# Kernel optimization log

Measured on AMD Instinct MI355X. Metric: run time of the kernel, lower is better.

The kernel has to match this reference:

```python
import jax, jax.numpy as jnp
import numpy as np

DIM = 512
HEADS = 4
HEAD_DIM = DIM // HEADS
HIDDEN = DIM * 2
DEPTH = 4
N = 32768
T = 4  # fixed branch/token dim


def _layernorm(x, w, b, eps=1e-5):
    m = jnp.mean(x, axis=-1, keepdims=True)
    v = jnp.mean(jnp.square(x - m), axis=-1, keepdims=True)
    return (x - m) * jax.lax.rsqrt(v + eps) * w + b


def setup_inputs() -> dict:
    key = jax.random.key(0)
    ks = jax.random.split(key, 24)
    s = 0.02
    d = {
        'x': jax.random.normal(ks[0], (N, DIM, T), dtype=jnp.float32),
        'branch_embed': s * jax.random.normal(ks[1], (T, DIM), dtype=jnp.float32),
        'ln1_w': jnp.ones((DEPTH, DIM), jnp.float32),
        'ln1_b': jnp.zeros((DEPTH, DIM), jnp.float32),
        'qkv_w': s * jax.random.normal(ks[2], (DEPTH, 3 * DIM, DIM), dtype=jnp.float32),
        'qkv_b': jnp.zeros((DEPTH, 3 * DIM), jnp.float32),
        'proj_w': s * jax.random.normal(ks[3], (DEPTH, DIM, DIM), dtype=jnp.float32),
        'proj_b': jnp.zeros((DEPTH, DIM), jnp.float32),
        'ln2_w': jnp.ones((DEPTH, DIM), jnp.float32),
        'ln2_b': jnp.zeros((DEPTH, DIM), jnp.float32),
        'ffn_w1': s * jax.random.normal(ks[4], (DEPTH, HIDDEN, DIM), dtype=jnp.float32),
        'ffn_b1': jnp.zeros((DEPTH, HIDDEN), jnp.float32),
        'ffn_w2': s * jax.random.normal(ks[5], (DEPTH, DIM, HIDDEN), dtype=jnp.float32),
        'ffn_b2': jnp.zeros((DEPTH, DIM), jnp.float32),
        'pool_q': s * jax.random.normal(ks[6], (DIM,), dtype=jnp.float32),
        'pool_w': s * jax.random.normal(ks[7], (DIM, DIM), dtype=jnp.float32),
        'out_ln_w': jnp.ones((DIM,), jnp.float32),
        'out_ln_b': jnp.zeros((DIM,), jnp.float32),
        'out_w1': s * jax.random.normal(ks[8], (DIM // 2, DIM), dtype=jnp.float32),
        'out_b1': jnp.zeros((DIM // 2,), jnp.float32),
        'out_w2': s * jax.random.normal(ks[9], (1, DIM // 2), dtype=jnp.float32),
        'out_b2': jnp.zeros((1,), jnp.float32),
    }
    return d


def reference(x, branch_embed, ln1_w, ln1_b, qkv_w, qkv_b, proj_w, proj_b,
              ln2_w, ln2_b, ffn_w1, ffn_b1, ffn_w2, ffn_b2,
              pool_q, pool_w, out_ln_w, out_ln_b, out_w1, out_b1, out_w2, out_b2):
    # (N, C, 4) -> (N, 4, C), add branch embedding
    x = jnp.swapaxes(x, 1, 2) + branch_embed[None]
    n = x.shape[0]
    scale = 1.0 / np.sqrt(HEAD_DIM)
    for i in range(DEPTH):
        # --- MHSA (pre-LN, eval mode -> dropout off) ---
        h = _layernorm(x, ln1_w[i], ln1_b[i])
        qkv = jnp.einsum('ntd,ed->nte', h, qkv_w[i]) + qkv_b[i]  # (N, T, 3D)
        q, k, v = jnp.split(qkv, 3, axis=-1)
        q = q.reshape(n, T, HEADS, HEAD_DIM).transpose(0, 2, 1, 3)
        k = k.reshape(n, T, HEADS, HEAD_DIM).transpose(0, 2, 1, 3)
        v = v.reshape(n, T, HEADS, HEAD_DIM).transpose(0, 2, 1, 3)
        scores = jnp.einsum('nhqd,nhkd->nhqk', q, k) * scale
        attn = jax.nn.softmax(scores, axis=-1)
        o = jnp.einsum('nhqk,nhkd->nhqd', attn, v)
        o = o.transpose(0, 2, 1, 3).reshape(n, T, DIM)
        o = jnp.einsum('ntd,ed->nte', o, proj_w[i]) + proj_b[i]
        x = x + o
        # --- FFN ---
        h = _layernorm(x, ln2_w[i], ln2_b[i])
        f = jax.nn.gelu(jnp.einsum('ntd,hd->nth', h, ffn_w1[i]) + ffn_b1[i], approximate=False)
        f = jnp.einsum('nth,dh->ntd', f, ffn_w2[i]) + ffn_b2[i]
        x = x + f
    # --- attention pooling head ---
    k = jnp.einsum('ntd,ed->nte', x, pool_w)            # pool_proj (no bias)
    score = jax.nn.softmax(jnp.einsum('d,ntd->nt', pool_q, k) / np.sqrt(DIM), axis=-1)
    z = jnp.einsum('nt,ntd->nd', score, x)
    z = _layernorm(z, out_ln_w, out_ln_b)
    z = jax.nn.gelu(z @ out_w1.T + out_b1, approximate=False)
    y = (z @ out_w2.T + out_b2)[:, 0]
    return y
```

## Files before the change

kernel.cpp:

```cpp
#include <hip/hip_runtime.h>

typedef unsigned short u16;
typedef unsigned int u32;
typedef __attribute__((ext_vector_type(8))) short s16x8;
typedef __attribute__((ext_vector_type(8))) unsigned short u16x8;
typedef __attribute__((ext_vector_type(4))) float f32x4;
typedef __attribute__((ext_vector_type(4))) unsigned int u32x4;

__device__ __forceinline__ u16 f2bf(float f) {
    u32 u = __float_as_uint(f);
    u32 r = (u + 0x7fffu + ((u >> 16) & 1u)) >> 16;
    return (u16)r;
}
__device__ __forceinline__ float bf2f(u16 u) { return __uint_as_float(((u32)u) << 16); }
__device__ __forceinline__ float bflo(u32 u) { return __uint_as_float(u << 16); }
__device__ __forceinline__ float bfhi(u32 u) { return __uint_as_float(u & 0xffff0000u); }
__device__ __forceinline__ float gelu_exact(float v) {
    return 0.5f * v * (1.0f + erff(v * 0.70710678118654752f));
}

__device__ __forceinline__ void gload16(const void* g, void* l) {
    __builtin_amdgcn_global_load_lds(
        (const __attribute__((address_space(1))) u32*)g,
        (__attribute__((address_space(3))) u32*)l, 16, 0, 0);
}

__global__ __launch_bounds__(256) void k_cvt6(const float* __restrict__ s0, u16* __restrict__ d0,
                                              const float* __restrict__ s1, u16* __restrict__ d1,
                                              const float* __restrict__ s2, u16* __restrict__ d2,
                                              const float* __restrict__ s3, u16* __restrict__ d3,
                                              const float* __restrict__ s4, u16* __restrict__ d4,
                                              const float* __restrict__ s5, u16* __restrict__ d5) {
    int i = blockIdx.x * 256 + threadIdx.x;
    const float* s; u16* d; int off;
    if (i < 786432)       { s = s0; d = d0; off = i; }
    else if (i < 1048576) { s = s1; d = d1; off = i - 786432; }
    else if (i < 1572864) { s = s2; d = d2; off = i - 1048576; }
    else if (i < 2097152) { s = s3; d = d3; off = i - 1572864; }
    else if (i < 2162688) { s = s4; d = d4; off = i - 2097152; }
    else                  { s = s5; d = d5; off = i - 2162688; }
    float4 v = *(const float4*)(s + (size_t)off * 4);
    u16 o0 = f2bf(v.x), o1 = f2bf(v.y), o2 = f2bf(v.z), o3 = f2bf(v.w);
    uint2 o; o.x = (u32)o0 | ((u32)o1 << 16); o.y = (u32)o2 | ((u32)o3 << 16);
    *(uint2*)(d + (size_t)off * 4) = o;
}

__global__ __launch_bounds__(256) void k_embed_ln(const float* __restrict__ x,
                                                  const float* __restrict__ be,
                                                  const float* __restrict__ w,
                                                  const float* __restrict__ b,
                                                  u16* __restrict__ Xb,
                                                  u16* __restrict__ Hb) {
    __shared__ u16 ld[4][512];
    int s = blockIdx.x;
    int tid = threadIdx.x;
    const float* xs = x + (size_t)s * 2048;
#pragma unroll
    for (int i = 0; i < 2; ++i) {
        int d = tid + i * 256;
        float4 v = *(const float4*)(xs + d * 4);
        ld[0][d] = f2bf(v.x + be[d]);
        ld[1][d] = f2bf(v.y + be[512 + d]);
        ld[2][d] = f2bf(v.z + be[1024 + d]);
        ld[3][d] = f2bf(v.w + be[1536 + d]);
    }
    __syncthreads();
    int t = tid >> 6, lane = tid & 63;
    u16x8 raw = *(const u16x8*)(&ld[t][lane * 8]);
    *(u16x8*)(Xb + ((size_t)s * 4 + t) * 512 + lane * 8) = raw;
    float a[8];
#pragma unroll
    for (int j = 0; j < 8; ++j) a[j] = bf2f(raw[j]);
    float s1 = 0.f, s2 = 0.f;
#pragma unroll
    for (int j = 0; j < 8; ++j) { s1 += a[j]; s2 += a[j] * a[j]; }
#pragma unroll
    for (int d = 1; d < 64; d <<= 1) { s1 += __shfl_xor(s1, d); s2 += __shfl_xor(s2, d); }
    float mean = s1 * (1.0f / 512.0f);
    float var  = s2 * (1.0f / 512.0f) - mean * mean;
    float rstd = rsqrtf(var + 1e-5f);
    float4 w0 = *(const float4*)(w + lane * 8);
    float4 w1 = *(const float4*)(w + lane * 8 + 4);
    float4 b0 = *(const float4*)(b + lane * 8);
    float4 b1 = *(const float4*)(b + lane * 8 + 4);
    float wv[8] = {w0.x, w0.y, w0.z, w0.w, w1.x, w1.y, w1.z, w1.w};
    float bv[8] = {b0.x, b0.y, b0.z, b0.w, b1.x, b1.y, b1.z, b1.w};
    u16x8 o;
#pragma unroll
    for (int j = 0; j < 8; ++j) o[j] = f2bf((a[j] - mean) * rstd * wv[j] + bv[j]);
    *(u16x8*)(Hb + ((size_t)s * 4 + t) * 512 + lane * 8) = o;
}

__global__ __launch_bounds__(256) void k_ln(const u16* __restrict__ Xb,
                                            const float* __restrict__ w,
                                            const float* __restrict__ b,
                                            u16* __restrict__ H) {
    int row = blockIdx.x * 4 + (threadIdx.x >> 6);
    int lane = threadIdx.x & 63;
    u16x8 xv = *(const u16x8*)(Xb + (size_t)row * 512 + lane * 8);
    float a[8];
#pragma unroll
    for (int j = 0; j < 8; ++j) a[j] = bf2f(xv[j]);
    float s1 = 0.f, s2 = 0.f;
#pragma unroll
    for (int j = 0; j < 8; ++j) { s1 += a[j]; s2 += a[j] * a[j]; }
#pragma unroll
    for (int d = 1; d < 64; d <<= 1) { s1 += __shfl_xor(s1, d); s2 += __shfl_xor(s2, d); }
    float mean = s1 * (1.0f / 512.0f);
    float var  = s2 * (1.0f / 512.0f) - mean * mean;
    float rstd = rsqrtf(var + 1e-5f);
    float4 w0 = *(const float4*)(w + lane * 8);
    float4 w1 = *(const float4*)(w + lane * 8 + 4);
    float4 b0 = *(const float4*)(b + lane * 8);
    float4 b1 = *(const float4*)(b + lane * 8 + 4);
    float wv[8] = {w0.x, w0.y, w0.z, w0.w, w1.x, w1.y, w1.z, w1.w};
    float bv[8] = {b0.x, b0.y, b0.z, b0.w, b1.x, b1.y, b1.z, b1.w};
    u16x8 o;
#pragma unroll
    for (int j = 0; j < 8; ++j) o[j] = f2bf((a[j] - mean) * rstd * wv[j] + bv[j]);
    *(u16x8*)(H + (size_t)row * 512 + lane * 8) = o;
}

template <bool BIAS, bool GELU_, bool RESID, bool BOUNCE, bool NT>
__global__ __launch_bounds__(512, 2) void k_gemm256(const u16* __restrict__ A,
                                                    const u16* __restrict__ W,
                                                    const float* __restrict__ bias,
                                                    u16* __restrict__ Cb,
                                                    u16* __restrict__ Xbres,
                                                    int K, int ncols, int TN, int T) {
    __shared__ __align__(16) u16 lds[2 * 32768];
    __shared__ __align__(16) u16 bounce[8192];
    int tid = threadIdx.x;
    int lane = tid & 63;
    int wid = tid >> 6;
    int G = gridDim.x, b = blockIdx.x;
    int start, end, step;
    if ((G & 7) == 0) {
        int xcd = b & 7, nxb = G >> 3, j = b >> 3;
        start = (int)(((long long)xcd * T) >> 3) + j;
        end   = (int)(((long long)(xcd + 1) * T) >> 3);
        step  = nxb;
    } else {
        start = (int)(((long long)b * T) / G);
        end   = (int)(((long long)(b + 1) * T) / G);
        step  = 1;
    }
    if (start >= end) return;
    int NS = K >> 6;
    int mgrp = wid >> 2, ngrp = wid & 3;

    f32x4 acc[8][4];
#pragma unroll
    for (int i = 0; i < 8; ++i)
#pragma unroll
        for (int j = 0; j < 4; ++j) acc[i][j] = (f32x4){0.f, 0.f, 0.f, 0.f};

    int srow = tid >> 3;
    int sel  = (((tid & 7) * 16) ^ ((srow & 7) << 4)) >> 1;
    size_t K64 = (size_t)K * 64;
    char* ldsB = (char*)lds;
    int wdst = wid * 1024;

    const u16 *cA0, *cA1, *cB0, *cB1, *nA0, *nA1, *nB0, *nB1;
    int cm0, cn0, nm0, nn0;
    auto tilePtrs = [&](int ti, const u16*& a0, const u16*& a1,
                        const u16*& b0, const u16*& b1, int& m0o, int& n0o) {
        int bx = ti / TN, by = ti - bx * TN;
        int m0 = bx * 256, n0 = by * 256;
        a0 = A + (size_t)(m0 + srow) * K + sel;
        a1 = A + (size_t)(m0 + 128 + srow) * K + sel;
        b0 = W + (size_t)(n0 + srow) * K + sel;
        b1 = W + (size_t)(n0 + 128 + srow) * K + sel;
        m0o = m0; n0o = n0;
    };

    auto S_Aq12 = [&](const u16* a0, const u16* a1, int s) {
        char* d = ldsB + (s & 1) * 65536 + wdst;
        gload16(a0 + (size_t)s * 64, d);
        gload16(a1 + (size_t)s * 64, d + 16384);
    };
    auto S_Aq34 = [&](const u16* a0, const u16* a1, int s) {
        char* d = ldsB + (s & 1) * 65536 + 8192 + wdst;
        gload16(a0 + K64 + (size_t)s * 64, d);
        gload16(a1 + K64 + (size_t)s * 64, d + 16384);
    };
    auto S_Blo = [&](const u16* b0, int s) {
        char* d = ldsB + (s & 1) * 65536 + 32768 + wdst;
        gload16(b0 + (size_t)s * 64, d);
        gload16(b0 + K64 + (size_t)s * 64, d + 8192);
    };
    auto S_Bhi = [&](const u16* b1, int s) {
        char* d = ldsB + (s & 1) * 65536 + 49152 + wdst;
        gload16(b1 + (size_t)s * 64, d);
        gload16(b1 + K64 + (size_t)s * 64, d + 8192);
    };

    int arow = mgrp * 128 + (lane & 15);
    int brow = ngrp * 64 + (lane & 15);
    int sub = (lane >> 4) << 4;
    int amask = ((arow & 7) << 4), bmask = ((brow & 7) << 4);
    int aoff0 = arow * 128 + (sub ^ amask);
    int boff0 = 32768 + brow * 128 + (sub ^ bmask);
    int aoff1 = arow * 128 + ((sub | 64) ^ amask);
    int boff1 = 32768 + brow * 128 + ((sub | 64) ^ bmask);

    tilePtrs(start, cA0, cA1, cB0, cB1, cm0, cn0);
    S_Blo(cB0, 0); S_Bhi(cB1, 0); S_Aq12(cA0, cA1, 0); S_Aq34(cA0, cA1, 0);
    S_Blo(cB0, 1); S_Bhi(cB1, 1); S_Aq12(cA0, cA1, 1);
    asm volatile("s_waitcnt vmcnt(6)" ::: "memory");
    __builtin_amdgcn_s_barrier();

    for (int ti = start; ti < end; ti += step) {
        bool hasNext = (ti + step < end);
        if (hasNext) tilePtrs(ti + step, nA0, nA1, nB0, nB1, nm0, nn0);

        s16x8 bfr[4][2];
        for (int s = 0; s < NS; ++s) {
            const char* sb = ldsB + (s & 1) * 65536;
            int st = s + 1, st2 = s + 2;
            bool n1 = st < NS, n2 = st2 < NS;
            s16x8 af[2][2];
#pragma unroll
            for (int ni = 0; ni < 4; ++ni) {
                bfr[ni][0] = *(const s16x8*)(sb + boff0 + ni * 2048);
                bfr[ni][1] = *(const s16x8*)(sb + boff1 + ni * 2048);
            }
            af[0][0] = *(const s16x8*)(sb + aoff0);
            af[0][1] = *(const s16x8*)(sb + aoff1);
            af[1][0] = *(const s16x8*)(sb + aoff0 + 2048);
            af[1][1] = *(const s16x8*)(sb + aoff1 + 2048);
            if (n1) S_Aq34(cA0, cA1, st); else if (hasNext) S_Aq34(nA0, nA1, st - NS);
            __builtin_amdgcn_s_barrier();
            __builtin_amdgcn_s_setprio(1);
#pragma unroll
            for (int mj = 0; mj < 2; ++mj)
#pragma unroll
                for (int ni = 0; ni < 4; ++ni) {
                    acc[mj][ni] = __builtin_amdgcn_mfma_f32_16x16x32_bf16(bfr[ni][0], af[mj][0], acc[mj][ni], 0, 0, 0);
                    acc[mj][ni] = __builtin_amdgcn_mfma_f32_16x16x32_bf16(bfr[ni][1], af[mj][1], acc[mj][ni], 0, 0, 0);
                }
            __builtin_amdgcn_s_setprio(0);
            __builtin_amdgcn_s_barrier();
#pragma unroll
            for (int mj = 0; mj < 2; ++mj) {
                af[mj][0] = *(const s16x8*)(sb + aoff0 + (2 + mj) * 2048);
                af[mj][1] = *(const s16x8*)(sb + aoff1 + (2 + mj) * 2048);
            }
            if (n2) S_Blo(cB0, st2); else if (hasNext) S_Blo(nB0, st2 - NS);
            __builtin_amdgcn_s_barrier();
            __builtin_amdgcn_s_setprio(1);
#pragma unroll
            for (int mj = 0; mj < 2; ++mj)
#pragma unroll
                for (int ni = 0; ni < 4; ++ni) {
                    acc[2 + mj][ni] = __builtin_amdgcn_mfma_f32_16x16x32_bf16(bfr[ni][0], af[mj][0], acc[2 + mj][ni], 0, 0, 0);
                    acc[2 + mj][ni] = __builtin_amdgcn_mfma_f32_16x16x32_bf16(bfr[ni][1], af[mj][1], acc[2 + mj][ni], 0, 0, 0);
                }
            __builtin_amdgcn_s_setprio(0);
            __builtin_amdgcn_s_barrier();
#pragma unroll
            for (int mj = 0; mj < 2; ++mj) {
                af[mj][0] = *(const s16x8*)(sb + aoff0 + (4 + mj) * 2048);
                af[mj][1] = *(const s16x8*)(sb + aoff1 + (4 + mj) * 2048);
            }
            if (n2) S_Bhi(cB1, st2); else if (hasNext) S_Bhi(nB1, st2 - NS);
            __builtin_amdgcn_s_barrier();
            __builtin_amdgcn_s_setprio(1);
#pragma unroll
            for (int mj = 0; mj < 2; ++mj)
#pragma unroll
                for (int ni = 0; ni < 4; ++ni) {
                    acc[4 + mj][ni] = __builtin_amdgcn_mfma_f32_16x16x32_bf16(bfr[ni][0], af[mj][0], acc[4 + mj][ni], 0, 0, 0);
                    acc[4 + mj][ni] = __builtin_amdgcn_mfma_f32_16x16x32_bf16(bfr[ni][1], af[mj][1], acc[4 + mj][ni], 0, 0, 0);
                }
            __builtin_amdgcn_s_setprio(0);
            __builtin_amdgcn_s_barrier();
#pragma unroll
            for (int mj = 0; mj < 2; ++mj) {
                af[mj][0] = *(const s16x8*)(sb + aoff0 + (6 + mj) * 2048);
                af[mj][1] = *(const s16x8*)(sb + aoff1 + (6 + mj) * 2048);
            }
            if (n2) S_Aq12(cA0, cA1, st2); else if (hasNext) S_Aq12(nA0, nA1, st2 - NS);
            __builtin_amdgcn_s_barrier();
            __builtin_amdgcn_s_setprio(1);
#pragma unroll
            for (int mj = 0; mj < 2; ++mj)
#pragma unroll
                for (int ni = 0; ni < 4; ++ni) {
                    acc[6 + mj][ni] = __builtin_amdgcn_mfma_f32_16x16x32_bf16(bfr[ni][0], af[mj][0], acc[6 + mj][ni], 0, 0, 0);
                    acc[6 + mj][ni] = __builtin_amdgcn_mfma_f32_16x16x32_bf16(bfr[ni][1], af[mj][1], acc[6 + mj][ni], 0, 0, 0);
                }
            __builtin_amdgcn_s_setprio(0);
            bool staged24 = n2 || hasNext;
            bool last = (s == NS - 1) && !hasNext;
            if (!last) {
                if (staged24) asm volatile("s_waitcnt vmcnt(6)" ::: "memory");
                else          asm volatile("s_waitcnt vmcnt(0)" ::: "memory");
                __builtin_amdgcn_s_barrier();
            }
        }

        int r_lane = lane & 15, cg = lane >> 4;
        float4 bb[4];
        if (BIAS) {
#pragma unroll
            for (int ni = 0; ni < 4; ++ni)
                bb[ni] = *(const float4*)(bias + cn0 + ngrp * 64 + ni * 16 + cg * 4);
        }
        if (BOUNCE) {
            u16* bw = bounce + wid * 1024;
            int qrow = lane >> 3, kc = lane & 7;
#pragma unroll
            for (int mi = 0; mi < 8; ++mi) {
                int rowbase = cm0 + mgrp * 128 + mi * 16;
#pragma unroll
                for (int ni = 0; ni < 4; ++ni) {
                    f32x4 v = acc[mi][ni];
                    if (BIAS) { v[0] += bb[ni].x; v[1] += bb[ni].y; v[2] += bb[ni].z; v[3] += bb[ni].w; }
                    if (GELU_) {
#pragma unroll
                        for (int j = 0; j < 4; ++j) v[j] = gelu_exact(v[j]);
                    }
                    uint2 o;
                    o.x = (u32)f2bf(v[0]) | ((u32)f2bf(v[1]) << 16);
                    o.y = (u32)f2bf(v[2]) | ((u32)f2bf(v[3]) << 16);
                    int slot = (4 * ni + cg) ^ (r_lane & 14);
                    *(uint2*)(bw + r_lane * 64 + slot * 4) = o;
                    acc[mi][ni] = (f32x4){0.f, 0.f, 0.f, 0.f};
                }
                asm volatile("s_waitcnt lgkmcnt(0)" ::: "memory");
#pragma unroll
                for (int h = 0; h < 2; ++h) {
                    int rd = h * 8 + qrow;
                    int e = (2 * kc) ^ (rd & 14);
                    u32x4 t = *(const u32x4*)(bw + rd * 64 + e * 4);
                    int row = rowbase + rd;
                    int c2 = cn0 + ngrp * 64 + kc * 8;
                    u16* dst = Cb + (size_t)row * ncols + c2;
                    if (NT) __builtin_nontemporal_store(t, (u32x4*)dst);
                    else    *(u32x4*)dst = t;
                }
                asm volatile("s_waitcnt lgkmcnt(0)" ::: "memory");
            }
        } else {
#pragma unroll
            for (int mi = 0; mi < 8; ++mi) {
                int row = cm0 + mgrp * 128 + mi * 16 + r_lane;
#pragma unroll
                for (int ni = 0; ni < 4; ++ni) {
                    int c = cn0 + ngrp * 64 + ni * 16 + cg * 4;
                    f32x4 v = acc[mi][ni];
                    if (BIAS) { v[0] += bb[ni].x; v[1] += bb[ni].y; v[2] += bb[ni].z; v[3] += bb[ni].w; }
                    if (GELU_) {
#pragma unroll
                        for (int j = 0; j < 4; ++j) v[j] = gelu_exact(v[j]);
                    }
                    if (RESID) {
                        u16* px = Xbres + (size_t)row * 512 + c;
                        uint2 xv = *(uint2*)px;
                        float x0 = bflo(xv.x) + v[0];
                        float x1 = bfhi(xv.x) + v[1];
                        float x2 = bflo(xv.y) + v[2];
                        float x3 = bfhi(xv.y) + v[3];
                        uint2 o;
                        o.x = (u32)f2bf(x0) | ((u32)f2bf(x1) << 16);
                        o.y = (u32)f2bf(x2) | ((u32)f2bf(x3) << 16);
                        *(uint2*)px = o;
                    } else {
                        u32 lo = (u32)f2bf(v[0]) | ((u32)f2bf(v[1]) << 16);
                        u32 hi = (u32)f2bf(v[2]) | ((u32)f2bf(v[3]) << 16);
                        uint2 o; o.x = lo; o.y = hi;
                        *(uint2*)(Cb + (size_t)row * ncols + c) = o;
                    }
                    acc[mi][ni] = (f32x4){0.f, 0.f, 0.f, 0.f};
                }
            }
        }
        cA0 = nA0; cA1 = nA1; cB0 = nB0; cB1 = nB1; cm0 = nm0; cn0 = nn0;
    }
}

__global__ __launch_bounds__(256) void k_attn(const u16* __restrict__ QKV, u16* __restrict__ O) {
    int task = blockIdx.x * 4 + (threadIdx.x >> 6);
    int lane = threadIdx.x & 63;
    int s = task >> 2, h = task & 3;
    const u16* base = QKV + (size_t)s * 4 * 1536 + h * 128;
    float q[4][2], k[4][2], v[4][2];
#pragma unroll
    for (int t = 0; t < 4; ++t) {
        const u16* row = base + t * 1536;
        u32 uq = *(const u32*)(row + lane * 2);
        u32 uk = *(const u32*)(row + 512 + lane * 2);
        u32 uv = *(const u32*)(row + 1024 + lane * 2);
        q[t][0] = bflo(uq); q[t][1] = bfhi(uq);
        k[t][0] = bflo(uk); k[t][1] = bfhi(uk);
        v[t][0] = bflo(uv); v[t][1] = bfhi(uv);
    }
    float sc[4][4];
#pragma unroll
    for (int i = 0; i < 4; ++i)
#pragma unroll
        for (int j = 0; j < 4; ++j) {
            float p = q[i][0] * k[j][0] + q[i][1] * k[j][1];
#pragma unroll
            for (int d = 1; d < 64; d <<= 1) p += __shfl_xor(p, d);
            sc[i][j] = p * 0.08838834764831845f;
        }
    float o[4][2];
#pragma unroll
    for (int i = 0; i < 4; ++i) {
        float mx = fmaxf(fmaxf(sc[i][0], sc[i][1]), fmaxf(sc[i][2], sc[i][3]));
        float e0 = expf(sc[i][0] - mx), e1 = expf(sc[i][1] - mx);
        float e2 = expf(sc[i][2] - mx), e3 = expf(sc[i][3] - mx);
        float inv = 1.0f / (e0 + e1 + e2 + e3);
        float a0 = e0 * inv, a1 = e1 * inv, a2 = e2 * inv, a3 = e3 * inv;
        o[i][0] = a0 * v[0][0] + a1 * v[1][0] + a2 * v[2][0] + a3 * v[3][0];
        o[i][1] = a0 * v[0][1] + a1 * v[1][1] + a2 * v[2][1] + a3 * v[3][1];
    }
#pragma unroll
    for (int i = 0; i < 4; ++i) {
        u32 pk = (u32)f2bf(o[i][0]) | ((u32)f2bf(o[i][1]) << 16);
        *(u32*)(O + ((size_t)s * 4 + i) * 512 + h * 128 + lane * 2) = pk;
    }
}

__global__ __launch_bounds__(256) void k_pool(const u16* __restrict__ Xb, const u16* __restrict__ Kp,
                                              const float* __restrict__ pq,
                                              const float* __restrict__ olnw, const float* __restrict__ olnb,
                                              u16* __restrict__ Zb) {
    int s = blockIdx.x * 4 + (threadIdx.x >> 6);
    int lane = threadIdx.x & 63;
    float4 p0 = *(const float4*)(pq + lane * 8);
    float4 p1 = *(const float4*)(pq + lane * 8 + 4);
    float pqv[8] = {p0.x, p0.y, p0.z, p0.w, p1.x, p1.y, p1.z, p1.w};
    float dot[4];
#pragma unroll
    for (int t = 0; t < 4; ++t) {
        u16x8 kv = *(const u16x8*)(Kp + ((size_t)s * 4 + t) * 512 + lane * 8);
        float p = 0.f;
#pragma unroll
        for (int j = 0; j < 8; ++j) p += pqv[j] * bf2f(kv[j]);
#pragma unroll
        for (int d = 1; d < 64; d <<= 1) p += __shfl_xor(p, d);
        dot[t] = p * 0.044194173824159216f;
    }
    float mx = fmaxf(fmaxf(dot[0], dot[1]), fmaxf(dot[2], dot[3]));
    float e[4], se = 0.f;
#pragma unroll
    for (int t = 0; t < 4; ++t) { e[t] = expf(dot[t] - mx); se += e[t]; }
    float inv = 1.0f / se;
    float z[8] = {0, 0, 0, 0, 0, 0, 0, 0};
#pragma unroll
    for (int t = 0; t < 4; ++t) {
        float scv = e[t] * inv;
        u16x8 xv = *(const u16x8*)(Xb + ((size_t)s * 4 + t) * 512 + lane * 8);
#pragma unroll
        for (int j = 0; j < 8; ++j) z[j] += scv * bf2f(xv[j]);
    }
    float s1 = 0.f, s2 = 0.f;
#pragma unroll
    for (int j = 0; j < 8; ++j) { s1 += z[j]; s2 += z[j] * z[j]; }
#pragma unroll
    for (int d = 1; d < 64; d <<= 1) { s1 += __shfl_xor(s1, d); s2 += __shfl_xor(s2, d); }
    float mean = s1 * (1.0f / 512.0f);
    float var  = s2 * (1.0f / 512.0f) - mean * mean;
    float rstd = rsqrtf(var + 1e-5f);
    float4 w0 = *(const float4*)(olnw + lane * 8);
    float4 w1 = *(const float4*)(olnw + lane * 8 + 4);
    float4 b0 = *(const float4*)(olnb + lane * 8);
    float4 b1 = *(const float4*)(olnb + lane * 8 + 4);
    float wv[8] = {w0.x, w0.y, w0.z, w0.w, w1.x, w1.y, w1.z, w1.w};
    float bv[8] = {b0.x, b0.y, b0.z, b0.w, b1.x, b1.y, b1.z, b1.w};
    u16x8 o;
#pragma unroll
    for (int j = 0; j < 8; ++j) o[j] = f2bf((z[j] - mean) * rstd * wv[j] + bv[j]);
    *(u16x8*)(Zb + (size_t)s * 512 + lane * 8) = o;
}

__global__ __launch_bounds__(256) void k_out2(const u16* __restrict__ G, const float* __restrict__ w2,
                                              const float* __restrict__ b2, float* __restrict__ y) {
    int s = blockIdx.x * 4 + (threadIdx.x >> 6);
    int lane = threadIdx.x & 63;
    uint2 u = *(const uint2*)(G + (size_t)s * 256 + lane * 4);
    float4 wv = *(const float4*)(w2 + lane * 4);
    float p = bflo(u.x) * wv.x + bfhi(u.x) * wv.y + bflo(u.y) * wv.z + bfhi(u.y) * wv.w;
#pragma unroll
    for (int d = 1; d < 64; d <<= 1) p += __shfl_xor(p, d);
    if (lane == 0) y[s] = p + b2[0];
}

extern "C" void kernel_launch(void* const* d_in, const int* in_sizes, int n_in,
                              void* d_out, int out_size, void* d_ws, size_t ws_size,
                              hipStream_t stream) {
    const float* x     = (const float*)d_in[0];
    const float* be    = (const float*)d_in[1];
    const float* ln1w  = (const float*)d_in[2];
    const float* ln1b  = (const float*)d_in[3];
    const float* qkvw  = (const float*)d_in[4];
    const float* qkvb  = (const float*)d_in[5];
    const float* projw = (const float*)d_in[6];
    const float* projb = (const float*)d_in[7];
    const float* ln2w  = (const float*)d_in[8];
    const float* ln2b  = (const float*)d_in[9];
    const float* f1w   = (const float*)d_in[10];
    const float* f1b   = (const float*)d_in[11];
    const float* f2w   = (const float*)d_in[12];
    const float* f2b   = (const float*)d_in[13];
    const float* poolq = (const float*)d_in[14];
    const float* poolw = (const float*)d_in[15];
    const float* olnw  = (const float*)d_in[16];
    const float* olnb  = (const float*)d_in[17];
    const float* ow1   = (const float*)d_in[18];
    const float* ob1   = (const float*)d_in[19];
    const float* ow2   = (const float*)d_in[20];
    const float* ob2   = (const float*)d_in[21];
    float* y = (float*)d_out;

    int N = in_sizes[0] / 2048;

    char* p = (char*)d_ws;
    auto take = [&](size_t b) { char* r = p; p += (b + 255) & ~(size_t)255; return r; };
    u16* qkvWb  = (u16*)take((size_t)3145728 * 2);
    u16* projWb = (u16*)take((size_t)1048576 * 2);
    u16* f1Wb   = (u16*)take((size_t)2097152 * 2);
    u16* f2Wb   = (u16*)take((size_t)2097152 * 2);
    u16* poolWb = (u16*)take((size_t)262144 * 2);
    u16* ow1b   = (u16*)take((size_t)131072 * 2);
    size_t fixedB = (size_t)(p - (char*)d_ws);

    int S = N;
    while (S > 256 && fixedB + (size_t)S * 20480 + 65536 > ws_size) S >>= 1;
    int R = S * 4;
    int TM = R / 256;

    u16* Xb    = (u16*)take((size_t)R * 512 * 2);
    u16* Hb    = (u16*)take((size_t)R * 512 * 2);
    u16* QKVb  = (u16*)take((size_t)R * 1536 * 2);
    u16* Kpb = QKVb;
    u16* Fb  = QKVb;
    u16* Gb  = (u16*)((char*)QKVb + (size_t)R * 512 * 2);
    u16* Zb  = Hb;

    k_cvt6<<<8576, 256, 0, stream>>>(qkvw, qkvWb, projw, projWb, f1w, f1Wb,
                                     f2w, f2Wb, poolw, poolWb, ow1, ow1b);

    auto gridFor = [](int T) { return T < 256 ? T : 256; };

    for (int c0 = 0; c0 < N; c0 += S) {
        const float* xin = x + (size_t)c0 * 2048;
        k_embed_ln<<<S, 256, 0, stream>>>(xin, be, ln1w, ln1b, Xb, Hb);
        for (int l = 0; l < 4; ++l) {
            if (l > 0)
                k_ln<<<R / 4, 256, 0, stream>>>(Xb, ln1w + l * 512, ln1b + l * 512, Hb);
            { int T = TM * 6;
              k_gemm256<true, false, false, true, true><<<gridFor(T), 512, 0, stream>>>(
                  Hb, qkvWb + (size_t)l * 786432, qkvb + l * 1536, QKVb, nullptr, 512, 1536, 6, T); }
            k_attn<<<S, 256, 0, stream>>>(QKVb, Hb);
            { int T = TM * 2;
              k_gemm256<true, false, true, false, false><<<gridFor(T), 512, 0, stream>>>(
                  Hb, projWb + (size_t)l * 262144, projb + l * 512, nullptr, Xb, 512, 512, 2, T); }
            k_ln<<<R / 4, 256, 0, stream>>>(Xb, ln2w + l * 512, ln2b + l * 512, Hb);
            { int T = TM * 4;
              k_gemm256<true, true, false, false, false><<<gridFor(T), 512, 0, stream>>>(
                  Hb, f1Wb + (size_t)l * 524288, f1b + l * 1024, Fb, nullptr, 512, 1024, 4, T); }
            { int T = TM * 2;
              k_gemm256<true, false, true, false, false><<<gridFor(T), 512, 0, stream>>>(
                  Fb, f2Wb + (size_t)l * 524288, f2b + l * 512, nullptr, Xb, 1024, 512, 2, T); }
        }
        { int T = TM * 2;
          k_gemm256<false, false, false, false, false><<<gridFor(T), 512, 0, stream>>>(
              Xb, poolWb, nullptr, Kpb, nullptr, 512, 512, 2, T); }
        k_pool<<<S / 4, 256, 0, stream>>>(Xb, Kpb, poolq, olnw, olnb, Zb);
        { int T = S / 256;
          k_gemm256<true, true, false, false, false><<<gridFor(T), 512, 0, stream>>>(
              Zb, ow1b, ob1, Gb, nullptr, 512, 256, 1, T); }
        k_out2<<<S / 4, 256, 0, stream>>>(Gb, ow2, ob2, y + c0);
    }
    (void)n_in; (void)out_size; (void)ws_size;
}
```

Measured before the change: 4.324 ms.

## Fuse LayerNorm into residual GEMM epilogues and fold pool projection into query

The residual-adding GEMMs (proj and FFN2) now compute the following LayerNorm in their epilogue. Each block handles both column tiles of a row band, accumulates per-row sums in shared memory, then writes the normalized rows, so the standalone LN kernels go away. The pooling projection is replaced algebraically by precomputing pool_q·W once, which removes a full GEMM over all tokens. The FFN1 GEMM also switches to the bounce/NT store path. The cost is a heavier epilogue with extra barriers and a second pass re-reading Xb, plus less scheduling freedom because tiles are paired.

```diff
diff --git a/kernel.cpp b/kernel.cpp
--- a/kernel.cpp
+++ b/kernel.cpp
@@ -25,24 +25,31 @@
         (__attribute__((address_space(3))) u32*)l, 16, 0, 0);
 }
 
-__global__ __launch_bounds__(256) void k_cvt6(const float* __restrict__ s0, u16* __restrict__ d0,
+__global__ __launch_bounds__(256) void k_cvt5(const float* __restrict__ s0, u16* __restrict__ d0,
                                               const float* __restrict__ s1, u16* __restrict__ d1,
                                               const float* __restrict__ s2, u16* __restrict__ d2,
                                               const float* __restrict__ s3, u16* __restrict__ d3,
-                                              const float* __restrict__ s4, u16* __restrict__ d4,
-                                              const float* __restrict__ s5, u16* __restrict__ d5) {
+                                              const float* __restrict__ s4, u16* __restrict__ d4) {
     int i = blockIdx.x * 256 + threadIdx.x;
     const float* s; u16* d; int off;
     if (i < 786432)       { s = s0; d = d0; off = i; }
     else if (i < 1048576) { s = s1; d = d1; off = i - 786432; }
     else if (i < 1572864) { s = s2; d = d2; off = i - 1048576; }
     else if (i < 2097152) { s = s3; d = d3; off = i - 1572864; }
-    else if (i < 2162688) { s = s4; d = d4; off = i - 2097152; }
-    else                  { s = s5; d = d5; off = i - 2162688; }
+    else                  { s = s4; d = d4; off = i - 2097152; }
     float4 v = *(const float4*)(s + (size_t)off * 4);
     u16 o0 = f2bf(v.x), o1 = f2bf(v.y), o2 = f2bf(v.z), o3 = f2bf(v.w);
     uint2 o; o.x = (u32)o0 | ((u32)o1 << 16); o.y = (u32)o2 | ((u32)o3 << 16);
     *(uint2*)(d + (size_t)off * 4) = o;
+}
+
+__global__ __launch_bounds__(256) void k_poolq(const float* __restrict__ pq,
+                                               const float* __restrict__ W,
+                                               float* __restrict__ qw) {
+    int d = blockIdx.x * 256 + threadIdx.x;
+    float s = 0.f;
+    for (int e = 0; e < 512; ++e) s += pq[e] * W[(size_t)e * 512 + d];
+    qw[d] = s;
 }
 
 __global__ __launch_bounds__(256) void k_embed_ln(const float* __restrict__ x,
@@ -91,42 +98,15 @@
     *(u16x8*)(Hb + ((size_t)s * 4 + t) * 512 + lane * 8) = o;
 }
 
-__global__ __launch_bounds__(256) void k_ln(const u16* __restrict__ Xb,
-                                            const float* __restrict__ w,
-                                            const float* __restrict__ b,
-                                            u16* __restrict__ H) {
-    int row = blockIdx.x * 4 + (threadIdx.x >> 6);
-    int lane = threadIdx.x & 63;
-    u16x8 xv = *(const u16x8*)(Xb + (size_t)row * 512 + lane * 8);
-    float a[8];
-#pragma unroll
-    for (int j = 0; j < 8; ++j) a[j] = bf2f(xv[j]);
-    float s1 = 0.f, s2 = 0.f;
-#pragma unroll
-    for (int j = 0; j < 8; ++j) { s1 += a[j]; s2 += a[j] * a[j]; }
-#pragma unroll
-    for (int d = 1; d < 64; d <<= 1) { s1 += __shfl_xor(s1, d); s2 += __shfl_xor(s2, d); }
-    float mean = s1 * (1.0f / 512.0f);
-    float var  = s2 * (1.0f / 512.0f) - mean * mean;
-    float rstd = rsqrtf(var + 1e-5f);
-    float4 w0 = *(const float4*)(w + lane * 8);
-    float4 w1 = *(const float4*)(w + lane * 8 + 4);
-    float4 b0 = *(const float4*)(b + lane * 8);
-    float4 b1 = *(const float4*)(b + lane * 8 + 4);
-    float wv[8] = {w0.x, w0.y, w0.z, w0.w, w1.x, w1.y, w1.z, w1.w};
-    float bv[8] = {b0.x, b0.y, b0.z, b0.w, b1.x, b1.y, b1.z, b1.w};
-    u16x8 o;
-#pragma unroll
-    for (int j = 0; j < 8; ++j) o[j] = f2bf((a[j] - mean) * rstd * wv[j] + bv[j]);
-    *(u16x8*)(H + (size_t)row * 512 + lane * 8) = o;
-}
-
-template <bool BIAS, bool GELU_, bool RESID, bool BOUNCE, bool NT>
+template <bool BIAS, bool GELU_, bool RESID, bool BOUNCE, bool NT, bool LNF>
 __global__ __launch_bounds__(512, 2) void k_gemm256(const u16* __restrict__ A,
                                                     const u16* __restrict__ W,
                                                     const float* __restrict__ bias,
                                                     u16* __restrict__ Cb,
                                                     u16* __restrict__ Xbres,
+                                                    const float* __restrict__ lnw,
+                                                    const float* __restrict__ lnb,
+                                                    u16* __restrict__ Hout,
                                                     int K, int ncols, int TN, int T) {
     __shared__ __align__(16) u16 lds[2 * 32768];
     __shared__ __align__(16) u16 bounce[8192];
@@ -134,18 +114,47 @@
     int lane = tid & 63;
     int wid = tid >> 6;
     int G = gridDim.x, b = blockIdx.x;
-    int start, end, step;
-    if ((G & 7) == 0) {
-        int xcd = b & 7, nxb = G >> 3, j = b >> 3;
-        start = (int)(((long long)xcd * T) >> 3) + j;
-        end   = (int)(((long long)(xcd + 1) * T) >> 3);
-        step  = nxb;
+    int startTi, ue = 0, ustep = 0, endT = 0, stepT = 0;
+    if (LNF) {
+        int U = T >> 1;
+        int us;
+        if ((G & 7) == 0) {
+            int xcd = b & 7, nxb = G >> 3, j = b >> 3;
+            us = (int)(((long long)xcd * U) >> 3) + j;
+            ue = (int)(((long long)(xcd + 1) * U) >> 3);
+            ustep = nxb;
+        } else {
+            us = (int)(((long long)b * U) / G);
+            ue = (int)(((long long)(b + 1) * U) / G);
+            ustep = 1;
+        }
+        if (us >= ue) return;
+        startTi = us * 2;
     } else {
-        start = (int)(((long long)b * T) / G);
-        end   = (int)(((long long)(b + 1) * T) / G);
-        step  = 1;
-    }
-    if (start >= end) return;
+        int st;
+        if ((G & 7) == 0) {
+            int xcd = b & 7, nxb = G >> 3, j = b >> 3;
+            st = (int)(((long long)xcd * T) >> 3) + j;
+            endT = (int)(((long long)(xcd + 1) * T) >> 3);
+            stepT = nxb;
+        } else {
+            st = (int)(((long long)b * T) / G);
+            endT = (int)(((long long)(b + 1) * T) / G);
+            stepT = 1;
+        }
+        if (st >= endT) return;
+        startTi = st;
+    }
+    auto nextOf = [&](int ti) -> int {
+        if (LNF) {
+            if (!(ti & 1)) return ti + 1;
+            int u = (ti >> 1) + ustep;
+            return u < ue ? u * 2 : -1;
+        } else {
+            int n = ti + stepT;
+            return n < endT ? n : -1;
+        }
+    };
     int NS = K >> 6;
     int mgrp = wid >> 2, ngrp = wid & 3;
 
@@ -204,15 +213,21 @@
     int aoff1 = arow * 128 + ((sub | 64) ^ amask);
     int boff1 = 32768 + brow * 128 + ((sub | 64) ^ bmask);
 
-    tilePtrs(start, cA0, cA1, cB0, cB1, cm0, cn0);
+    if (LNF) {
+        *((float4*)bounce + tid) = (float4){0.f, 0.f, 0.f, 0.f};
+    }
+
+    tilePtrs(startTi, cA0, cA1, cB0, cB1, cm0, cn0);
     S_Blo(cB0, 0); S_Bhi(cB1, 0); S_Aq12(cA0, cA1, 0); S_Aq34(cA0, cA1, 0);
     S_Blo(cB0, 1); S_Bhi(cB1, 1); S_Aq12(cA0, cA1, 1);
     asm volatile("s_waitcnt vmcnt(6)" ::: "memory");
     __builtin_amdgcn_s_barrier();
 
-    for (int ti = start; ti < end; ti += step) {
-        bool hasNext = (ti + step < end);
-        if (hasNext) tilePtrs(ti + step, nA0, nA1, nB0, nB1, nm0, nn0);
+    int ti = startTi;
+    while (true) {
+        int tnext = nextOf(ti);
+        bool hasNext = tnext >= 0;
+        if (hasNext) tilePtrs(tnext, nA0, nA1, nB0, nB1, nm0, nn0);
 
         s16x8 bfr[4][2];
         for (int s = 0; s < NS; ++s) {
@@ -307,7 +322,105 @@
             for (int ni = 0; ni < 4; ++ni)
                 bb[ni] = *(const float4*)(bias + cn0 + ngrp * 64 + ni * 16 + cg * 4);
         }
-        if (BOUNCE) {
+        if (LNF) {
+            float* pS = (float*)bounce;
+            bool half1 = (ti & 1) != 0;
+#pragma unroll
+            for (int mi = 0; mi < 8; ++mi) {
+                int lrow = mgrp * 128 + mi * 16 + r_lane;
+                int row = cm0 + lrow;
+                float s1 = 0.f, s2 = 0.f;
+#pragma unroll
+                for (int ni = 0; ni < 4; ++ni) {
+                    int c = cn0 + ngrp * 64 + ni * 16 + cg * 4;
+                    f32x4 v = acc[mi][ni];
+                    if (BIAS) { v[0] += bb[ni].x; v[1] += bb[ni].y; v[2] += bb[ni].z; v[3] += bb[ni].w; }
+                    u16* px = Xbres + (size_t)row * 512 + c;
+                    uint2 xv = *(uint2*)px;
+                    float x0 = bflo(xv.x) + v[0];
+                    float x1 = bfhi(xv.x) + v[1];
+                    float x2 = bflo(xv.y) + v[2];
+                    float x3 = bfhi(xv.y) + v[3];
+                    uint2 o;
+                    o.x = (u32)f2bf(x0) | ((u32)f2bf(x1) << 16);
+                    o.y = (u32)f2bf(x2) | ((u32)f2bf(x3) << 16);
+                    *(uint2*)px = o;
+                    float r0 = bflo(o.x), r1 = bfhi(o.x), r2 = bflo(o.y), r3 = bfhi(o.y);
+                    s1 += r0 + r1 + r2 + r3;
+                    s2 += r0 * r0 + r1 * r1 + r2 * r2 + r3 * r3;
+                    if (half1) acc[mi][ni] = (f32x4){r0, r1, r2, r3};
+                    else       acc[mi][ni] = (f32x4){0.f, 0.f, 0.f, 0.f};
+                }
+                s1 += __shfl_xor(s1, 16); s2 += __shfl_xor(s2, 16);
+                s1 += __shfl_xor(s1, 32); s2 += __shfl_xor(s2, 32);
+                if (cg == 0) {
+                    float* p = pS + ((ngrp << 8) + lrow) * 2;
+                    p[0] += s1; p[1] += s2;
+                }
+            }
+            if (half1) {
+                __syncthreads();
+                float mean[8], rstd[8];
+#pragma unroll
+                for (int mi = 0; mi < 8; ++mi) {
+                    int lrow = mgrp * 128 + mi * 16 + r_lane;
+                    float t1 = 0.f, t2 = 0.f;
+#pragma unroll
+                    for (int g = 0; g < 4; ++g) {
+                        float2 pv = *(float2*)(pS + ((g << 8) + lrow) * 2);
+                        t1 += pv.x; t2 += pv.y;
+                    }
+                    float m = t1 * (1.0f / 512.0f);
+                    mean[mi] = m;
+                    rstd[mi] = rsqrtf(t2 * (1.0f / 512.0f) - m * m + 1e-5f);
+                }
+#pragma unroll
+                for (int mi = 0; mi < 8; ++mi) {
+                    int row = cm0 + mgrp * 128 + mi * 16 + r_lane;
+#pragma unroll
+                    for (int ni = 0; ni < 4; ++ni) {
+                        int c = 256 + ngrp * 64 + ni * 16 + cg * 4;
+                        float4 wv = *(const float4*)(lnw + c);
+                        float4 bv = *(const float4*)(lnb + c);
+                        f32x4 v = acc[mi][ni];
+                        uint2 o;
+                        o.x = (u32)f2bf((v[0] - mean[mi]) * rstd[mi] * wv.x + bv.x)
+                            | ((u32)f2bf((v[1] - mean[mi]) * rstd[mi] * wv.y + bv.y) << 16);
+                        o.y = (u32)f2bf((v[2] - mean[mi]) * rstd[mi] * wv.z + bv.z)
+                            | ((u32)f2bf((v[3] - mean[mi]) * rstd[mi] * wv.w + bv.w) << 16);
+                        *(uint2*)(Hout + (size_t)row * 512 + c) = o;
+                        acc[mi][ni] = (f32x4){0.f, 0.f, 0.f, 0.f};
+                    }
+                }
+#pragma unroll
+                for (int mi = 0; mi < 8; ++mi) {
+                    int row = cm0 + mgrp * 128 + mi * 16 + r_lane;
+#pragma unroll
+                    for (int ni = 0; ni < 4; ++ni) {
+                        int c = ngrp * 64 + ni * 16 + cg * 4;
+                        uint2 xv = *(const uint2*)(Xbres + (size_t)row * 512 + c);
+                        float4 wv = *(const float4*)(lnw + c);
+                        float4 bv = *(const float4*)(lnb + c);
+                        float r0 = bflo(xv.x), r1 = bfhi(xv.x), r2 = bflo(xv.y), r3 = bfhi(xv.y);
+                        uint2 o;
+                        o.x = (u32)f2bf((r0 - mean[mi]) * rstd[mi] * wv.x + bv.x)
+                            | ((u32)f2bf((r1 - mean[mi]) * rstd[mi] * wv.y + bv.y) << 16);
+                        o.y = (u32)f2bf((r2 - mean[mi]) * rstd[mi] * wv.z + bv.z)
+                            | ((u32)f2bf((r3 - mean[mi]) * rstd[mi] * wv.w + bv.w) << 16);
+                        *(uint2*)(Hout + (size_t)row * 512 + c) = o;
+                    }
+                }
+                __syncthreads();
+                if (cg == 0) {
+#pragma unroll
+                    for (int mi = 0; mi < 8; ++mi) {
+                        int lrow = mgrp * 128 + mi * 16 + r_lane;
+                        float* p = pS + ((ngrp << 8) + lrow) * 2;
+                        p[0] = 0.f; p[1] = 0.f;
+                    }
+                }
+            }
+        } else if (BOUNCE) {
             u16* bw = bounce + wid * 1024;
             int qrow = lane >> 3, kc = lane & 7;
 #pragma unroll
@@ -376,7 +489,9 @@
                 }
             }
         }
+        if (!hasNext) break;
         cA0 = nA0; cA1 = nA1; cB0 = nB0; cB1 = nB1; cm0 = nm0; cn0 = nn0;
+        ti = tnext;
     }
 }
 
@@ -424,22 +539,22 @@
     }
 }
 
-__global__ __launch_bounds__(256) void k_pool(const u16* __restrict__ Xb, const u16* __restrict__ Kp,
-                                              const float* __restrict__ pq,
+__global__ __launch_bounds__(256) void k_pool(const u16* __restrict__ Xb, const float* __restrict__ qw,
                                               const float* __restrict__ olnw, const float* __restrict__ olnb,
                                               u16* __restrict__ Zb) {
     int s = blockIdx.x * 4 + (threadIdx.x >> 6);
     int lane = threadIdx.x & 63;
-    float4 p0 = *(const float4*)(pq + lane * 8);
-    float4 p1 = *(const float4*)(pq + lane * 8 + 4);
-    float pqv[8] = {p0.x, p0.y, p0.z, p0.w, p1.x, p1.y, p1.z, p1.w};
+    float4 q0 = *(const float4*)(qw + lane * 8);
+    float4 q1 = *(const float4*)(qw + lane * 8 + 4);
+    float qv[8] = {q0.x, q0.y, q0.z, q0.w, q1.x, q1.y, q1.z, q1.w};
+    u16x8 xr[4];
     float dot[4];
 #pragma unroll
     for (int t = 0; t < 4; ++t) {
-        u16x8 kv = *(const u16x8*)(Kp + ((size_t)s * 4 + t) * 512 + lane * 8);
+        xr[t] = *(const u16x8*)(Xb + ((size_t)s * 4 + t) * 512 + lane * 8);
         float p = 0.f;
 #pragma unroll
-        for (int j = 0; j < 8; ++j) p += pqv[j] * bf2f(kv[j]);
+        for (int j = 0; j < 8; ++j) p += qv[j] * bf2f(xr[t][j]);
 #pragma unroll
         for (int d = 1; d < 64; d <<= 1) p += __shfl_xor(p, d);
         dot[t] = p * 0.044194173824159216f;
@@ -453,9 +568,8 @@
 #pragma unroll
     for (int t = 0; t < 4; ++t) {
         float scv = e[t] * inv;
-        u16x8 xv = *(const u16x8*)(Xb + ((size_t)s * 4 + t) * 512 + lane * 8);
-#pragma unroll
-        for (int j = 0; j < 8; ++j) z[j] += scv * bf2f(xv[j]);
+#pragma unroll
+        for (int j = 0; j < 8; ++j) z[j] += scv * bf2f(xr[t][j]);
     }
     float s1 = 0.f, s2 = 0.f;
 #pragma unroll
@@ -524,8 +638,8 @@
     u16* projWb = (u16*)take((size_t)1048576 * 2);
     u16* f1Wb   = (u16*)take((size_t)2097152 * 2);
     u16* f2Wb   = (u16*)take((size_t)2097152 * 2);
-    u16* poolWb = (u16*)take((size_t)262144 * 2);
     u16* ow1b   = (u16*)take((size_t)131072 * 2);
+    float* qw   = (float*)take(512 * 4);
     size_t fixedB = (size_t)(p - (char*)d_ws);
 
     int S = N;
@@ -536,13 +650,13 @@
     u16* Xb    = (u16*)take((size_t)R * 512 * 2);
     u16* Hb    = (u16*)take((size_t)R * 512 * 2);
     u16* QKVb  = (u16*)take((size_t)R * 1536 * 2);
-    u16* Kpb = QKVb;
     u16* Fb  = QKVb;
     u16* Gb  = (u16*)((char*)QKVb + (size_t)R * 512 * 2);
     u16* Zb  = Hb;
 
-    k_cvt6<<<8576, 256, 0, stream>>>(qkvw, qkvWb, projw, projWb, f1w, f1Wb,
-                                     f2w, f2Wb, poolw, poolWb, ow1, ow1b);
+    k_cvt5<<<8320, 256, 0, stream>>>(qkvw, qkvWb, projw, projWb, f1w, f1Wb,
+                                     f2w, f2Wb, ow1, ow1b);
+    k_poolq<<<2, 256, 0, stream>>>(poolq, poolw, qw);
 
     auto gridFor = [](int T) { return T < 256 ? T : 256; };
 
@@ -550,30 +664,35 @@
         const float* xin = x + (size_t)c0 * 2048;
         k_embed_ln<<<S, 256, 0, stream>>>(xin, be, ln1w, ln1b, Xb, Hb);
         for (int l = 0; l < 4; ++l) {
-            if (l > 0)
-                k_ln<<<R / 4, 256, 0, stream>>>(Xb, ln1w + l * 512, ln1b + l * 512, Hb);
             { int T = TM * 6;
-              k_gemm256<true, false, false, true, true><<<gridFor(T), 512, 0, stream>>>(
-                  Hb, qkvWb + (size_t)l * 786432, qkvb + l * 1536, QKVb, nullptr, 512, 1536, 6, T); }
+              k_gemm256<true, false, false, true, true, false><<<gridFor(T), 512, 0, stream>>>(
+                  Hb, qkvWb + (size_t)l * 786432, qkvb + l * 1536, QKVb, nullptr,
+                  nullptr, nullptr, nullptr, 512, 1536, 6, T); }
             k_attn<<<S, 256, 0, stream>>>(QKVb, Hb);
             { int T = TM * 2;
-              k_gemm256<true, false, true, false, false><<<gridFor(T), 512, 0, stream>>>(
-                  Hb, projWb + (size_t)l * 262144, projb + l * 512, nullptr, Xb, 512, 512, 2, T); }
-            k_ln<<<R / 4, 256, 0, stream>>>(Xb, ln2w + l * 512, ln2b + l * 512, Hb);
+              k_gemm256<true, false, true, false, false, true><<<gridFor(T), 512, 0, stream>>>(
+                  Hb, projWb + (size_t)l * 262144, projb + l * 512, nullptr, Xb,
+                  ln2w + l * 512, ln2b + l * 512, Hb, 512, 512, 2, T); }
             { int T = TM * 4;
-              k_gemm256<true, true, false, false, false><<<gridFor(T), 512, 0, stream>>>(
-                  Hb, f1Wb + (size_t)l * 524288, f1b + l * 1024, Fb, nullptr, 512, 1024, 4, T); }
-            { int T = TM * 2;
-              k_gemm256<true, false, true, false, false><<<gridFor(T), 512, 0, stream>>>(
-                  Fb, f2Wb + (size_t)l * 524288, f2b + l * 512, nullptr, Xb, 1024, 512, 2, T); }
-        }
-        { int T = TM * 2;
-          k_gemm256<false, false, false, false, false><<<gridFor(T), 512, 0, stream>>>(
-              Xb, poolWb, nullptr, Kpb, nullptr, 512, 512, 2, T); }
-        k_pool<<<S / 4, 256, 0, stream>>>(Xb, Kpb, poolq, olnw, olnb, Zb);
+              k_gemm256<true, true, false, true, true, false><<<gridFor(T), 512, 0, stream>>>(
+                  Hb, f1Wb + (size_t)l * 524288, f1b + l * 1024, Fb, nullptr,
+                  nullptr, nullptr, nullptr, 512, 1024, 4, T); }
+            if (l < 3) {
+                int T = TM * 2;
+                k_gemm256<true, false, true, false, false, true><<<gridFor(T), 512, 0, stream>>>(
+                    Fb, f2Wb + (size_t)l * 524288, f2b + l * 512, nullptr, Xb,
+                    ln1w + (l + 1) * 512, ln1b + (l + 1) * 512, Hb, 1024, 512, 2, T);
+            } else {
+                int T = TM * 2;
+                k_gemm256<true, false, true, false, false, false><<<gridFor(T), 512, 0, stream>>>(
+                    Fb, f2Wb + (size_t)l * 524288, f2b + l * 512, nullptr, Xb,
+                    nullptr, nullptr, nullptr, 1024, 512, 2, T);
+            }
+        }
+        k_pool<<<S / 4, 256, 0, stream>>>(Xb, qw, olnw, olnb, Zb);
         { int T = S / 256;
-          k_gemm256<true, true, false, false, false><<<gridFor(T), 512, 0, stream>>>(
-              Zb, ow1b, ob1, Gb, nullptr, 512, 256, 1, T); }
+          k_gemm256<true, true, false, false, false, false><<<gridFor(T), 512, 0, stream>>>(
+              Zb, ow1b, ob1, Gb, nullptr, nullptr, nullptr, nullptr, 512, 256, 1, T); }
         k_out2<<<S / 4, 256, 0, stream>>>(Gb, ow2, ob2, y + c0);
     }
     (void)n_in; (void)out_size; (void)ws_size;
```

Result: slower. 4.676 ms (+8.1%).
